# Kernel optimization log

Measured on AMD Instinct MI355X. Metric: run time of the kernel, lower is better.

## Reference

```python
import jax, jax.numpy as jnp
import numpy as np

NUM_HEADS = 8


def _mc_linear(x, W, b):
    # Per-channel linear over the feature (h) dim.
    # x: (b,c,h,w), W: (c,f,h), b: (c,f,1) -> (b,c,f,w)
    return jnp.einsum('bchw,cfh->bcfw', x, W) + b


def setup_inputs() -> dict:
    key = jax.random.key(0)
    ks = jax.random.split(key, 9)
    b, c, f, w = 2, 8, 256, 1024
    s = 1.0 / np.sqrt(f).astype(np.float32)
    d = {'x': jax.random.normal(ks[0], (b, c, f, w), jnp.float32)}
    for i, name in enumerate(['q', 'k', 'v', 'o']):
        d['W' + name] = jax.random.normal(ks[1 + 2 * i], (c, f, f), jnp.float32) * s
        d['b' + name] = jax.random.normal(ks[2 + 2 * i], (c, f, 1), jnp.float32) * 0.01
    return d


def reference(x, Wq, bq, Wk, bk, Wv, bv, Wo, bo):
    b, c, h, w = x.shape
    hd = h // NUM_HEADS
    # projections -> (b,c,f,w), then to (b,c,heads,w,hd) / (b,c,heads,hd,w)
    q = _mc_linear(x, Wq, bq).transpose(0, 1, 3, 2).reshape(b, c, w, NUM_HEADS, hd).transpose(0, 1, 3, 2, 4)
    k = _mc_linear(x, Wk, bk).transpose(0, 1, 3, 2).reshape(b, c, w, NUM_HEADS, hd).transpose(0, 1, 3, 4, 2)
    v = _mc_linear(x, Wv, bv).transpose(0, 1, 3, 2).reshape(b, c, w, NUM_HEADS, hd).transpose(0, 1, 3, 2, 4)
    qk = jnp.matmul(q, k) / jnp.sqrt(jnp.asarray(h, x.dtype))  # (b,c,heads,w,w); note scale uses h, per source
    a = jnp.matmul(jax.nn.softmax(qk, axis=-1), v)             # (b,c,heads,w,hd)
    a = a.transpose(0, 1, 3, 2, 4).reshape(b, c, w, h).transpose(0, 1, 3, 2)  # (b,c,h,w)
    out = _mc_linear(a, Wo, bo)
    return out, qk
```

## Files before the change

kernel.cpp:

```cpp
#include <hip/hip_runtime.h>
#include <hip/hip_bf16.h>

#define BC 16
#define HH 256
#define WW 1024
#define NH 8
#define HD 32
#define SST 68

typedef __attribute__((ext_vector_type(8))) short bf16x8;
typedef __attribute__((ext_vector_type(4))) float f32x4;

static __device__ __forceinline__ unsigned short f2bu(float f) {
    __hip_bfloat16 h = __float2bfloat16(f);
    unsigned short r;
    __builtin_memcpy(&r, &h, 2);
    return r;
}

__global__ __launch_bounds__(256) void cast_fused(
    const float* __restrict__ x, __hip_bfloat16* __restrict__ xT,
    const float* __restrict__ w0, const float* __restrict__ w1,
    const float* __restrict__ w2, const float* __restrict__ w3,
    __hip_bfloat16* __restrict__ o0, __hip_bfloat16* __restrict__ o1,
    __hip_bfloat16* __restrict__ o2, __hip_bfloat16* __restrict__ o3) {
    if (blockIdx.z == 16) {
        const float* src = w0;
        __hip_bfloat16* dst = o0;
        if (blockIdx.y == 1) { src = w1; dst = o1; }
        else if (blockIdx.y == 2) { src = w2; dst = o2; }
        else if (blockIdx.y == 3) { src = w3; dst = o3; }
        const int base = blockIdx.x * 256 + threadIdx.x;
#pragma unroll
        for (int i = 0; i < 32; ++i) {
            const long t = (long)base + (long)i * 4096;
            float4 v = ((const float4*)src)[t];
            ushort4 o = make_ushort4(f2bu(v.x), f2bu(v.y), f2bu(v.z), f2bu(v.w));
            ((ushort4*)dst)[t] = o;
        }
        return;
    }
    __shared__ float tile[64][65];
    const int bc = blockIdx.z;
    const int h0 = blockIdx.y * 64, w0t = blockIdx.x * 64;
    const int tx = threadIdx.x & 63, ty = threadIdx.x >> 6;
    const float* xp = x + ((long)bc * HH + h0) * WW + w0t;
    for (int r = ty; r < 64; r += 4)
        tile[r][tx] = xp[(long)r * WW + tx];
    __syncthreads();
    __hip_bfloat16* xo = xT + ((long)bc * WW + w0t) * HH + h0;
    for (int r = ty; r < 64; r += 4)
        xo[(long)r * HH + tx] = __float2bfloat16(tile[tx][r]);
}

template <int MI, int NI, int OUTF32>
static __device__ __forceinline__ void gemm_body(
    const __hip_bfloat16* __restrict__ Ap, int lda,
    const __hip_bfloat16* __restrict__ Bp, int ldb,
    char* __restrict__ Cp, int ldc,
    const float* __restrict__ bp, int biasMode, int m0, int n0, int lane) {
    const int lr = lane & 15, kl = (lane >> 4) * 8;

    const __hip_bfloat16* ap = Ap + (long)(m0 + lr) * lda + kl;
    const __hip_bfloat16* bpp = Bp + (long)(n0 + lr) * ldb + kl;

    f32x4 acc[MI][NI] = {};
    bf16x8 afA[MI], bfA[NI], afB[MI], bfB[NI];
#pragma unroll
    for (int i = 0; i < MI; ++i) afA[i] = *(const bf16x8*)(ap + (long)i * 16 * lda);
#pragma unroll
    for (int j = 0; j < NI; ++j) bfA[j] = *(const bf16x8*)(bpp + (long)j * 16 * ldb);

#pragma unroll
    for (int kk = 0; kk < 8; ++kk) {
        const int kn = (kk + 1) * 32;
        if ((kk & 1) == 0) {
            if (kn < HH) {
#pragma unroll
                for (int i = 0; i < MI; ++i)
                    afB[i] = *(const bf16x8*)(ap + (long)i * 16 * lda + kn);
#pragma unroll
                for (int j = 0; j < NI; ++j)
                    bfB[j] = *(const bf16x8*)(bpp + (long)j * 16 * ldb + kn);
            }
#pragma unroll
            for (int i = 0; i < MI; ++i)
#pragma unroll
                for (int j = 0; j < NI; ++j)
                    acc[i][j] = __builtin_amdgcn_mfma_f32_16x16x32_bf16(
                        afA[i], bfA[j], acc[i][j], 0, 0, 0);
        } else {
            if (kn < HH) {
#pragma unroll
                for (int i = 0; i < MI; ++i)
                    afA[i] = *(const bf16x8*)(ap + (long)i * 16 * lda + kn);
#pragma unroll
                for (int j = 0; j < NI; ++j)
                    bfA[j] = *(const bf16x8*)(bpp + (long)j * 16 * ldb + kn);
            }
#pragma unroll
            for (int i = 0; i < MI; ++i)
#pragma unroll
                for (int j = 0; j < NI; ++j)
                    acc[i][j] = __builtin_amdgcn_mfma_f32_16x16x32_bf16(
                        afB[i], bfB[j], acc[i][j], 0, 0, 0);
        }
    }

    const int col0 = lane & 15;
    const int rowg = (lane >> 4) * 4;
#pragma unroll
    for (int i = 0; i < MI; ++i) {
#pragma unroll
        for (int j = 0; j < NI; ++j) {
            const int n = n0 + j * 16 + col0;
            float addc = 0.0f;
            if (biasMode == 2) addc = bp[n];
#pragma unroll
            for (int r = 0; r < 4; ++r) {
                const int m = m0 + i * 16 + rowg + r;
                float v = acc[i][j][r] + ((biasMode == 1) ? bp[m] : addc);
                if (OUTF32)
                    ((float*)Cp)[(long)m * ldc + n] = v;
                else
                    ((__hip_bfloat16*)Cp)[(long)m * ldc + n] = __float2bfloat16(v);
            }
        }
    }
}

__global__ __launch_bounds__(256, 3) void gemm_qkv(
    const __hip_bfloat16* __restrict__ xT,
    const __hip_bfloat16* __restrict__ wqb, const __hip_bfloat16* __restrict__ wkb,
    const __hip_bfloat16* __restrict__ wvb,
    __hip_bfloat16* __restrict__ Qt, __hip_bfloat16* __restrict__ Kt,
    __hip_bfloat16* __restrict__ Vm,
    const float* __restrict__ bq, const float* __restrict__ bk,
    const float* __restrict__ bv) {
    const int bc = blockIdx.z, ch = bc & 7, y = blockIdx.y;
    const int wave = threadIdx.x >> 6, lane = threadIdx.x & 63;
    const __hip_bfloat16* xb = xT + (long)bc * WW * HH;

    if (y < 2) {
        const __hip_bfloat16* wb = ((y == 0) ? wqb : wkb) + (long)ch * HH * HH;
        __hip_bfloat16* Cb = ((y == 0) ? Qt : Kt) + (long)bc * WW * HH;
        const float* bp = ((y == 0) ? bq : bk) + ch * HH;
        const int bm = (blockIdx.x >> 1) * 128, bn = (blockIdx.x & 1) * 128;
        const int m0 = bm + (wave >> 1) * 64, n0 = bn + (wave & 1) * 64;
        gemm_body<4, 4, 0>(xb, HH, wb, HH, (char*)Cb, HH, bp, 2, m0, n0, lane);
    } else {
        const __hip_bfloat16* wb = wvb + (long)ch * HH * HH;
        __hip_bfloat16* Cb = Vm + (long)bc * HH * WW;
        const float* bp = bv + ch * HH;
        const int bm = (blockIdx.x >> 3) * 128, bn = (blockIdx.x & 7) * 128;
        const int m0 = bm + (wave >> 1) * 64, n0 = bn + (wave & 1) * 64;
        gemm_body<4, 4, 0>(wb, HH, xb, HH, (char*)Cb, WW, bp, 1, m0, n0, lane);
    }
}

__global__ __launch_bounds__(256, 2) void gemm_o(
    const __hip_bfloat16* __restrict__ wob, const __hip_bfloat16* __restrict__ At,
    float* __restrict__ out, const float* __restrict__ bo) {
    const int bc = blockIdx.z, ch = bc & 7;
    const int wave = threadIdx.x >> 6, lane = threadIdx.x & 63;
    const __hip_bfloat16* wb = wob + (long)ch * HH * HH;
    const __hip_bfloat16* ab = At + (long)bc * WW * HH;
    float* Cb = out + (long)bc * HH * WW;
    const float* bp = bo + ch * HH;
    const int bm = (blockIdx.x >> 4) * 128, bn = (blockIdx.x & 15) * 64;
    const int m0 = bm + (wave >> 1) * 64, n0 = bn + (wave & 1) * 32;
    gemm_body<4, 2, 1>(wb, HH, ab, HH, (char*)Cb, WW, bp, 1, m0, n0, lane);
}

static __device__ __forceinline__ void attn_body(
    const bf16x8 (&kc)[4], const bf16x8 (&vc)[2][2],
    bf16x8 (&kn)[4], bf16x8 (&vn)[2][2], bool pre, int wj,
    const bf16x8 (&qf)[2], float* __restrict__ sl, float* __restrict__ qkp,
    const __hip_bfloat16* __restrict__ Kb, const __hip_bfloat16* __restrict__ Vb,
    f32x4 (&oacc)[2][2], float (&lacc)[2],
    int lr, int g, int kl, int rowg) {
    const f32x4 zf = {0.0f, 0.0f, 0.0f, 0.0f};
    f32x4 s[2][4];
#pragma unroll
    for (int mf = 0; mf < 2; ++mf)
#pragma unroll
        for (int nf = 0; nf < 4; ++nf)
            s[mf][nf] = __builtin_amdgcn_mfma_f32_16x16x32_bf16(
                qf[mf], kc[nf], zf, 0, 0, 0);

#pragma unroll
    for (int mf = 0; mf < 2; ++mf)
#pragma unroll
        for (int nf = 0; nf < 4; ++nf) {
            s[mf][nf] *= 0.0625f;
#pragma unroll
            for (int r = 0; r < 4; ++r)
                sl[(mf * 16 + rowg + r) * SST + nf * 16 + lr] = s[mf][nf][r];
        }

    f32x4 sd[8];
#pragma unroll
    for (int st = 0; st < 8; ++st)
        sd[st] = *(const f32x4*)(sl + (st * 4 + g) * SST + lr * 4);

    if (pre) {
#pragma unroll
        for (int nf = 0; nf < 4; ++nf)
            kn[nf] = *(const bf16x8*)(Kb + (long)(wj + 64 + nf * 16 + lr) * HH);
#pragma unroll
        for (int ks = 0; ks < 2; ++ks)
#pragma unroll
            for (int nf = 0; nf < 2; ++nf)
                vn[ks][nf] = *(const bf16x8*)(Vb + (long)(nf * 16 + lr) * WW +
                                              wj + 64 + ks * 32 + kl);
    }

#pragma unroll
    for (int st = 0; st < 8; ++st)
        __builtin_nontemporal_store(
            sd[st], (f32x4*)(qkp + (long)(st * 4 + g) * WW + wj + lr * 4));

#pragma unroll
    for (int ks = 0; ks < 2; ++ks) {
        bf16x8 pf[2];
#pragma unroll
        for (int mf = 0; mf < 2; ++mf) {
            const float* sr = sl + (mf * 16 + lr) * SST + ks * 32 + kl;
            f32x4 a = *(const f32x4*)(sr);
            f32x4 b = *(const f32x4*)(sr + 4);
            float p[8];
#pragma unroll
            for (int j = 0; j < 4; ++j) p[j] = __expf(a[j]);
#pragma unroll
            for (int j = 0; j < 4; ++j) p[4 + j] = __expf(b[j]);
            float sum = 0.0f;
            bf16x8 pv;
#pragma unroll
            for (int j = 0; j < 8; ++j) {
                sum += p[j];
                pv[j] = (short)f2bu(p[j]);
            }
            lacc[mf] += sum;
            pf[mf] = pv;
        }
#pragma unroll
        for (int mf = 0; mf < 2; ++mf)
#pragma unroll
            for (int nf = 0; nf < 2; ++nf)
                oacc[mf][nf] = __builtin_amdgcn_mfma_f32_16x16x32_bf16(
                    pf[mf], vc[ks][nf], oacc[mf][nf], 0, 0, 0);
    }
}

__global__ __launch_bounds__(256) void attn_fused(
    const __hip_bfloat16* __restrict__ Qt, const __hip_bfloat16* __restrict__ Kt,
    const __hip_bfloat16* __restrict__ Vm, float* __restrict__ qk_out,
    __hip_bfloat16* __restrict__ At) {
    __shared__ float S_lds[4][32 * SST];
    const int bc = blockIdx.z, head = blockIdx.y;
    const int wave = threadIdx.x >> 6, lane = threadIdx.x & 63;
    const int wi0 = blockIdx.x * 128 + wave * 32;
    const int lr = lane & 15, g = lane >> 4, kl = g * 8;
    const int rowg = g * 4;

    const __hip_bfloat16* Qb = Qt + (long)bc * WW * HH;
    bf16x8 qf[2];
#pragma unroll
    for (int mf = 0; mf < 2; ++mf)
        qf[mf] = *(const bf16x8*)(Qb + (long)(wi0 + mf * 16 + lr) * HH + head * HD + kl);

    const __hip_bfloat16* Kb = Kt + (long)bc * WW * HH + head * HD + kl;
    const __hip_bfloat16* Vb = Vm + ((long)bc * HH + head * HD) * WW;
    float* qkp = qk_out + (((long)bc * NH + head) * WW + wi0) * WW;

    f32x4 oacc[2][2] = {};
    float lacc[2] = {0.0f, 0.0f};
    float* sl = &S_lds[wave][0];

    bf16x8 kfA[4], kfB[4], vfA[2][2], vfB[2][2];
#pragma unroll
    for (int nf = 0; nf < 4; ++nf)
        kfA[nf] = *(const bf16x8*)(Kb + (long)(nf * 16 + lr) * HH);
#pragma unroll
    for (int ks = 0; ks < 2; ++ks)
#pragma unroll
        for (int nf = 0; nf < 2; ++nf)
            vfA[ks][nf] = *(const bf16x8*)(Vb + (long)(nf * 16 + lr) * WW +
                                           ks * 32 + kl);

    for (int it = 0; it < 8; ++it) {
        const int wj0 = it * 128;
        attn_body(kfA, vfA, kfB, vfB, true, wj0,
                  qf, sl, qkp, Kb, Vb, oacc, lacc, lr, g, kl, rowg);
        attn_body(kfB, vfB, kfA, vfA, (it < 7), wj0 + 64,
                  qf, sl, qkp, Kb, Vb, oacc, lacc, lr, g, kl, rowg);
    }

#pragma unroll
    for (int mf = 0; mf < 2; ++mf) {
        lacc[mf] += __shfl_xor(lacc[mf], 16);
        lacc[mf] += __shfl_xor(lacc[mf], 32);
    }
    float linv[2][4];
#pragma unroll
    for (int mf = 0; mf < 2; ++mf)
#pragma unroll
        for (int r = 0; r < 4; ++r)
            linv[mf][r] = 1.0f / __shfl(lacc[mf], rowg + r);

    __hip_bfloat16* Ao = At + (long)bc * WW * HH;
#pragma unroll
    for (int mf = 0; mf < 2; ++mf)
#pragma unroll
        for (int nf = 0; nf < 2; ++nf)
#pragma unroll
            for (int r = 0; r < 4; ++r) {
                float v = oacc[mf][nf][r] * linv[mf][r];
                Ao[(long)(wi0 + mf * 16 + rowg + r) * HH + head * HD + nf * 16 + lr] =
                    __float2bfloat16(v);
            }
}

extern "C" void kernel_launch(void* const* d_in, const int* in_sizes, int n_in,
                              void* d_out, int out_size, void* d_ws, size_t ws_size,
                              hipStream_t stream) {
    const float* x  = (const float*)d_in[0];
    const float* Wq = (const float*)d_in[1];
    const float* bq = (const float*)d_in[2];
    const float* Wk = (const float*)d_in[3];
    const float* bk = (const float*)d_in[4];
    const float* Wv = (const float*)d_in[5];
    const float* bv = (const float*)d_in[6];
    const float* Wo = (const float*)d_in[7];
    const float* bo = (const float*)d_in[8];

    float* out = (float*)d_out;
    float* qk  = out + (long)BC * HH * WW;

    char* ws = (char*)d_ws;
    __hip_bfloat16* xT  = (__hip_bfloat16*)(ws);
    __hip_bfloat16* wqb = (__hip_bfloat16*)(ws + 8388608);
    __hip_bfloat16* wkb = (__hip_bfloat16*)(ws + 9437184);
    __hip_bfloat16* wvb = (__hip_bfloat16*)(ws + 10485760);
    __hip_bfloat16* wob = (__hip_bfloat16*)(ws + 11534336);
    __hip_bfloat16* Qt  = (__hip_bfloat16*)(ws + 12582912);
    __hip_bfloat16* Kt  = (__hip_bfloat16*)(ws + 20971520);
    __hip_bfloat16* Vm  = (__hip_bfloat16*)(ws + 29360128);
    __hip_bfloat16* At  = (__hip_bfloat16*)(ws + 37748736);

    cast_fused<<<dim3(16, 4, 17), 256, 0, stream>>>(
        x, xT, Wq, Wk, Wv, Wo, wqb, wkb, wvb, wob);

    gemm_qkv<<<dim3(16, 3, BC), 256, 0, stream>>>(
        xT, wqb, wkb, wvb, Qt, Kt, Vm, bq, bk, bv);

    attn_fused<<<dim3(8, NH, BC), 256, 0, stream>>>(Qt, Kt, Vm, qk, At);

    gemm_o<<<dim3(32, 1, BC), 256, 0, stream>>>(wob, At, out, bo);

    (void)in_sizes; (void)n_in; (void)out_size; (void)ws_size;
}
```

Measured before the change: 190.4 us.

## Fold softmax scale into Wq, store bf16 P to LDS, vectorize transpose

```diff
diff --git a/kernel.cpp b/kernel.cpp
--- a/kernel.cpp
+++ b/kernel.cpp
@@ -6,7 +6,7 @@
 #define WW 1024
 #define NH 8
 #define HD 32
-#define SST 68
+#define PST 72
 
 typedef __attribute__((ext_vector_type(8))) short bf16x8;
 typedef __attribute__((ext_vector_type(4))) float f32x4;
@@ -27,15 +27,17 @@
     if (blockIdx.z == 16) {
         const float* src = w0;
         __hip_bfloat16* dst = o0;
-        if (blockIdx.y == 1) { src = w1; dst = o1; }
-        else if (blockIdx.y == 2) { src = w2; dst = o2; }
-        else if (blockIdx.y == 3) { src = w3; dst = o3; }
+        float wscale = 0.0625f;
+        if (blockIdx.y == 1) { src = w1; dst = o1; wscale = 1.0f; }
+        else if (blockIdx.y == 2) { src = w2; dst = o2; wscale = 1.0f; }
+        else if (blockIdx.y == 3) { src = w3; dst = o3; wscale = 1.0f; }
         const int base = blockIdx.x * 256 + threadIdx.x;
 #pragma unroll
         for (int i = 0; i < 32; ++i) {
             const long t = (long)base + (long)i * 4096;
             float4 v = ((const float4*)src)[t];
-            ushort4 o = make_ushort4(f2bu(v.x), f2bu(v.y), f2bu(v.z), f2bu(v.w));
+            ushort4 o = make_ushort4(f2bu(v.x * wscale), f2bu(v.y * wscale),
+                                     f2bu(v.z * wscale), f2bu(v.w * wscale));
             ((ushort4*)dst)[t] = o;
         }
         return;
@@ -43,14 +45,27 @@
     __shared__ float tile[64][65];
     const int bc = blockIdx.z;
     const int h0 = blockIdx.y * 64, w0t = blockIdx.x * 64;
-    const int tx = threadIdx.x & 63, ty = threadIdx.x >> 6;
     const float* xp = x + ((long)bc * HH + h0) * WW + w0t;
-    for (int r = ty; r < 64; r += 4)
-        tile[r][tx] = xp[(long)r * WW + tx];
+    const int w4 = threadIdx.x & 15, hr = threadIdx.x >> 4;
+#pragma unroll
+    for (int p = 0; p < 4; ++p) {
+        const int h = hr + p * 16;
+        float4 v = *(const float4*)(xp + (long)h * WW + w4 * 4);
+        tile[h][w4 * 4 + 0] = v.x;
+        tile[h][w4 * 4 + 1] = v.y;
+        tile[h][w4 * 4 + 2] = v.z;
+        tile[h][w4 * 4 + 3] = v.w;
+    }
     __syncthreads();
     __hip_bfloat16* xo = xT + ((long)bc * WW + w0t) * HH + h0;
-    for (int r = ty; r < 64; r += 4)
-        xo[(long)r * HH + tx] = __float2bfloat16(tile[tx][r]);
+    const int hq = threadIdx.x & 15, wq = threadIdx.x >> 4;
+#pragma unroll
+    for (int p = 0; p < 4; ++p) {
+        const int w = wq + p * 16;
+        ushort4 o = make_ushort4(f2bu(tile[hq * 4 + 0][w]), f2bu(tile[hq * 4 + 1][w]),
+                                 f2bu(tile[hq * 4 + 2][w]), f2bu(tile[hq * 4 + 3][w]));
+        *(ushort4*)(xo + (long)w * HH + hq * 4) = o;
+    }
 }
 
 template <int MI, int NI, int OUTF32>
@@ -58,7 +73,8 @@
     const __hip_bfloat16* __restrict__ Ap, int lda,
     const __hip_bfloat16* __restrict__ Bp, int ldb,
     char* __restrict__ Cp, int ldc,
-    const float* __restrict__ bp, int biasMode, int m0, int n0, int lane) {
+    const float* __restrict__ bp, int biasMode, float bmul,
+    int m0, int n0, int lane) {
     const int lr = lane & 15, kl = (lane >> 4) * 8;
 
     const __hip_bfloat16* ap = Ap + (long)(m0 + lr) * lda + kl;
@@ -115,7 +131,7 @@
         for (int j = 0; j < NI; ++j) {
             const int n = n0 + j * 16 + col0;
             float addc = 0.0f;
-            if (biasMode == 2) addc = bp[n];
+            if (biasMode == 2) addc = bp[n] * bmul;
 #pragma unroll
             for (int r = 0; r < 4; ++r) {
                 const int m = m0 + i * 16 + rowg + r;
@@ -145,16 +161,17 @@
         const __hip_bfloat16* wb = ((y == 0) ? wqb : wkb) + (long)ch * HH * HH;
         __hip_bfloat16* Cb = ((y == 0) ? Qt : Kt) + (long)bc * WW * HH;
         const float* bp = ((y == 0) ? bq : bk) + ch * HH;
+        const float bmul = (y == 0) ? 0.0625f : 1.0f;
         const int bm = (blockIdx.x >> 1) * 128, bn = (blockIdx.x & 1) * 128;
         const int m0 = bm + (wave >> 1) * 64, n0 = bn + (wave & 1) * 64;
-        gemm_body<4, 4, 0>(xb, HH, wb, HH, (char*)Cb, HH, bp, 2, m0, n0, lane);
+        gemm_body<4, 4, 0>(xb, HH, wb, HH, (char*)Cb, HH, bp, 2, bmul, m0, n0, lane);
     } else {
         const __hip_bfloat16* wb = wvb + (long)ch * HH * HH;
         __hip_bfloat16* Cb = Vm + (long)bc * HH * WW;
         const float* bp = bv + ch * HH;
         const int bm = (blockIdx.x >> 3) * 128, bn = (blockIdx.x & 7) * 128;
         const int m0 = bm + (wave >> 1) * 64, n0 = bn + (wave & 1) * 64;
-        gemm_body<4, 4, 0>(wb, HH, xb, HH, (char*)Cb, WW, bp, 1, m0, n0, lane);
+        gemm_body<4, 4, 0>(wb, HH, xb, HH, (char*)Cb, WW, bp, 1, 1.0f, m0, n0, lane);
     }
 }
 
@@ -169,15 +186,16 @@
     const float* bp = bo + ch * HH;
     const int bm = (blockIdx.x >> 4) * 128, bn = (blockIdx.x & 15) * 64;
     const int m0 = bm + (wave >> 1) * 64, n0 = bn + (wave & 1) * 32;
-    gemm_body<4, 2, 1>(wb, HH, ab, HH, (char*)Cb, WW, bp, 1, m0, n0, lane);
+    gemm_body<4, 2, 1>(wb, HH, ab, HH, (char*)Cb, WW, bp, 1, 1.0f, m0, n0, lane);
 }
 
 static __device__ __forceinline__ void attn_body(
     const bf16x8 (&kc)[4], const bf16x8 (&vc)[2][2],
     bf16x8 (&kn)[4], bf16x8 (&vn)[2][2], bool pre, int wj,
-    const bf16x8 (&qf)[2], float* __restrict__ sl, float* __restrict__ qkp,
+    const bf16x8 (&qf)[2], __hip_bfloat16* __restrict__ pl,
+    float* __restrict__ qkp,
     const __hip_bfloat16* __restrict__ Kb, const __hip_bfloat16* __restrict__ Vb,
-    f32x4 (&oacc)[2][2], float (&lacc)[2],
+    f32x4 (&oacc)[2][2], float (&lacc)[2][4],
     int lr, int g, int kl, int rowg) {
     const f32x4 zf = {0.0f, 0.0f, 0.0f, 0.0f};
     f32x4 s[2][4];
@@ -188,21 +206,6 @@
             s[mf][nf] = __builtin_amdgcn_mfma_f32_16x16x32_bf16(
                 qf[mf], kc[nf], zf, 0, 0, 0);
 
-#pragma unroll
-    for (int mf = 0; mf < 2; ++mf)
-#pragma unroll
-        for (int nf = 0; nf < 4; ++nf) {
-            s[mf][nf] *= 0.0625f;
-#pragma unroll
-            for (int r = 0; r < 4; ++r)
-                sl[(mf * 16 + rowg + r) * SST + nf * 16 + lr] = s[mf][nf][r];
-        }
-
-    f32x4 sd[8];
-#pragma unroll
-    for (int st = 0; st < 8; ++st)
-        sd[st] = *(const f32x4*)(sl + (st * 4 + g) * SST + lr * 4);
-
     if (pre) {
 #pragma unroll
         for (int nf = 0; nf < 4; ++nf)
@@ -216,33 +219,34 @@
     }
 
 #pragma unroll
-    for (int st = 0; st < 8; ++st)
-        __builtin_nontemporal_store(
-            sd[st], (f32x4*)(qkp + (long)(st * 4 + g) * WW + wj + lr * 4));
+    for (int mf = 0; mf < 2; ++mf)
+#pragma unroll
+        for (int r = 0; r < 4; ++r) {
+            float* qr = qkp + (long)(mf * 16 + rowg + r) * WW + wj + lr;
+#pragma unroll
+            for (int nf = 0; nf < 4; ++nf)
+                __builtin_nontemporal_store(s[mf][nf][r], qr + nf * 16);
+        }
+
+#pragma unroll
+    for (int mf = 0; mf < 2; ++mf) {
+        __hip_bfloat16* pw = pl + (long)(mf * 16 + rowg) * PST + lr;
+#pragma unroll
+        for (int nf = 0; nf < 4; ++nf)
+#pragma unroll
+            for (int r = 0; r < 4; ++r) {
+                float p = __expf(s[mf][nf][r]);
+                lacc[mf][r] += p;
+                pw[r * PST + nf * 16] = __float2bfloat16(p);
+            }
+    }
 
 #pragma unroll
     for (int ks = 0; ks < 2; ++ks) {
         bf16x8 pf[2];
 #pragma unroll
-        for (int mf = 0; mf < 2; ++mf) {
-            const float* sr = sl + (mf * 16 + lr) * SST + ks * 32 + kl;
-            f32x4 a = *(const f32x4*)(sr);
-            f32x4 b = *(const f32x4*)(sr + 4);
-            float p[8];
-#pragma unroll
-            for (int j = 0; j < 4; ++j) p[j] = __expf(a[j]);
-#pragma unroll
-            for (int j = 0; j < 4; ++j) p[4 + j] = __expf(b[j]);
-            float sum = 0.0f;
-            bf16x8 pv;
-#pragma unroll
-            for (int j = 0; j < 8; ++j) {
-                sum += p[j];
-                pv[j] = (short)f2bu(p[j]);
-            }
-            lacc[mf] += sum;
-            pf[mf] = pv;
-        }
+        for (int mf = 0; mf < 2; ++mf)
+            pf[mf] = *(const bf16x8*)(pl + (long)(mf * 16 + lr) * PST + ks * 32 + kl);
 #pragma unroll
         for (int mf = 0; mf < 2; ++mf)
 #pragma unroll
@@ -256,7 +260,7 @@
     const __hip_bfloat16* __restrict__ Qt, const __hip_bfloat16* __restrict__ Kt,
     const __hip_bfloat16* __restrict__ Vm, float* __restrict__ qk_out,
     __hip_bfloat16* __restrict__ At) {
-    __shared__ float S_lds[4][32 * SST];
+    __shared__ __hip_bfloat16 P_lds[4][32 * PST];
     const int bc = blockIdx.z, head = blockIdx.y;
     const int wave = threadIdx.x >> 6, lane = threadIdx.x & 63;
     const int wi0 = blockIdx.x * 128 + wave * 32;
@@ -274,8 +278,8 @@
     float* qkp = qk_out + (((long)bc * NH + head) * WW + wi0) * WW;
 
     f32x4 oacc[2][2] = {};
-    float lacc[2] = {0.0f, 0.0f};
-    float* sl = &S_lds[wave][0];
+    float lacc[2][4] = {};
+    __hip_bfloat16* pl = &P_lds[wave][0];
 
     bf16x8 kfA[4], kfB[4], vfA[2][2], vfB[2][2];
 #pragma unroll
@@ -291,22 +295,23 @@
     for (int it = 0; it < 8; ++it) {
         const int wj0 = it * 128;
         attn_body(kfA, vfA, kfB, vfB, true, wj0,
-                  qf, sl, qkp, Kb, Vb, oacc, lacc, lr, g, kl, rowg);
+                  qf, pl, qkp, Kb, Vb, oacc, lacc, lr, g, kl, rowg);
         attn_body(kfB, vfB, kfA, vfA, (it < 7), wj0 + 64,
-                  qf, sl, qkp, Kb, Vb, oacc, lacc, lr, g, kl, rowg);
-    }
-
-#pragma unroll
-    for (int mf = 0; mf < 2; ++mf) {
-        lacc[mf] += __shfl_xor(lacc[mf], 16);
-        lacc[mf] += __shfl_xor(lacc[mf], 32);
-    }
+                  qf, pl, qkp, Kb, Vb, oacc, lacc, lr, g, kl, rowg);
+    }
+
     float linv[2][4];
 #pragma unroll
     for (int mf = 0; mf < 2; ++mf)
 #pragma unroll
-        for (int r = 0; r < 4; ++r)
-            linv[mf][r] = 1.0f / __shfl(lacc[mf], rowg + r);
+        for (int r = 0; r < 4; ++r) {
+            float v = lacc[mf][r];
+            v += __shfl_xor(v, 1);
+            v += __shfl_xor(v, 2);
+            v += __shfl_xor(v, 4);
+            v += __shfl_xor(v, 8);
+            linv[mf][r] = 1.0f / v;
+        }
 
     __hip_bfloat16* Ao = At + (long)bc * WW * HH;
 #pragma unroll
```

Result: slower. 200.7 us (+5.4%).

## Fuse fp32-to-bf16 casts into GEMM fragment loads and drop cast kernel

Applied to the files above, without the earlier changes.

```diff
diff --git a/kernel.cpp b/kernel.cpp
--- a/kernel.cpp
+++ b/kernel.cpp
@@ -18,58 +18,46 @@
     return r;
 }
 
-__global__ __launch_bounds__(256) void cast_fused(
-    const float* __restrict__ x, __hip_bfloat16* __restrict__ xT,
-    const float* __restrict__ w0, const float* __restrict__ w1,
-    const float* __restrict__ w2, const float* __restrict__ w3,
-    __hip_bfloat16* __restrict__ o0, __hip_bfloat16* __restrict__ o1,
-    __hip_bfloat16* __restrict__ o2, __hip_bfloat16* __restrict__ o3) {
-    if (blockIdx.z == 16) {
-        const float* src = w0;
-        __hip_bfloat16* dst = o0;
-        if (blockIdx.y == 1) { src = w1; dst = o1; }
-        else if (blockIdx.y == 2) { src = w2; dst = o2; }
-        else if (blockIdx.y == 3) { src = w3; dst = o3; }
-        const int base = blockIdx.x * 256 + threadIdx.x;
-#pragma unroll
-        for (int i = 0; i < 32; ++i) {
-            const long t = (long)base + (long)i * 4096;
-            float4 v = ((const float4*)src)[t];
-            ushort4 o = make_ushort4(f2bu(v.x), f2bu(v.y), f2bu(v.z), f2bu(v.w));
-            ((ushort4*)dst)[t] = o;
-        }
-        return;
-    }
-    __shared__ float tile[64][65];
-    const int bc = blockIdx.z;
-    const int h0 = blockIdx.y * 64, w0t = blockIdx.x * 64;
-    const int tx = threadIdx.x & 63, ty = threadIdx.x >> 6;
-    const float* xp = x + ((long)bc * HH + h0) * WW + w0t;
-    for (int r = ty; r < 64; r += 4)
-        tile[r][tx] = xp[(long)r * WW + tx];
-    __syncthreads();
-    __hip_bfloat16* xo = xT + ((long)bc * WW + w0t) * HH + h0;
-    for (int r = ty; r < 64; r += 4)
-        xo[(long)r * HH + tx] = __float2bfloat16(tile[tx][r]);
-}
-
-template <int MI, int NI, int OUTF32>
+template <int LK>
+static __device__ __forceinline__ bf16x8 load_frag(
+    const void* __restrict__ p, long row, int k, int ld, float scale) {
+    bf16x8 r;
+    if constexpr (LK == 0) {
+        r = *(const bf16x8*)((const __hip_bfloat16*)p + row * (long)ld + k);
+    } else if constexpr (LK == 1) {
+        const float* f = (const float*)p + row * (long)ld + k;
+        float4 a = *(const float4*)f;
+        float4 b = *(const float4*)(f + 4);
+        r[0] = (short)f2bu(a.x * scale); r[1] = (short)f2bu(a.y * scale);
+        r[2] = (short)f2bu(a.z * scale); r[3] = (short)f2bu(a.w * scale);
+        r[4] = (short)f2bu(b.x * scale); r[5] = (short)f2bu(b.y * scale);
+        r[6] = (short)f2bu(b.z * scale); r[7] = (short)f2bu(b.w * scale);
+    } else {
+        const float* f = (const float*)p + row + (long)k * ld;
+#pragma unroll
+        for (int j = 0; j < 8; ++j)
+            r[j] = (short)f2bu(f[(long)j * ld]);
+    }
+    return r;
+}
+
+template <int MI, int NI, int OUTF32, int LKA, int LKB>
 static __device__ __forceinline__ void gemm_body(
-    const __hip_bfloat16* __restrict__ Ap, int lda,
-    const __hip_bfloat16* __restrict__ Bp, int ldb,
+    const void* __restrict__ Ap, int lda, float asc,
+    const void* __restrict__ Bp, int ldb, float bsc,
     char* __restrict__ Cp, int ldc,
-    const float* __restrict__ bp, int biasMode, int m0, int n0, int lane) {
+    const float* __restrict__ bp, int biasMode, float bmul,
+    int m0, int n0, int lane) {
     const int lr = lane & 15, kl = (lane >> 4) * 8;
-
-    const __hip_bfloat16* ap = Ap + (long)(m0 + lr) * lda + kl;
-    const __hip_bfloat16* bpp = Bp + (long)(n0 + lr) * ldb + kl;
 
     f32x4 acc[MI][NI] = {};
     bf16x8 afA[MI], bfA[NI], afB[MI], bfB[NI];
 #pragma unroll
-    for (int i = 0; i < MI; ++i) afA[i] = *(const bf16x8*)(ap + (long)i * 16 * lda);
-#pragma unroll
-    for (int j = 0; j < NI; ++j) bfA[j] = *(const bf16x8*)(bpp + (long)j * 16 * ldb);
+    for (int i = 0; i < MI; ++i)
+        afA[i] = load_frag<LKA>(Ap, m0 + i * 16 + lr, kl, lda, asc);
+#pragma unroll
+    for (int j = 0; j < NI; ++j)
+        bfA[j] = load_frag<LKB>(Bp, n0 + j * 16 + lr, kl, ldb, bsc);
 
 #pragma unroll
     for (int kk = 0; kk < 8; ++kk) {
@@ -78,10 +66,10 @@
             if (kn < HH) {
 #pragma unroll
                 for (int i = 0; i < MI; ++i)
-                    afB[i] = *(const bf16x8*)(ap + (long)i * 16 * lda + kn);
+                    afB[i] = load_frag<LKA>(Ap, m0 + i * 16 + lr, kl + kn, lda, asc);
 #pragma unroll
                 for (int j = 0; j < NI; ++j)
-                    bfB[j] = *(const bf16x8*)(bpp + (long)j * 16 * ldb + kn);
+                    bfB[j] = load_frag<LKB>(Bp, n0 + j * 16 + lr, kl + kn, ldb, bsc);
             }
 #pragma unroll
             for (int i = 0; i < MI; ++i)
@@ -93,10 +81,10 @@
             if (kn < HH) {
 #pragma unroll
                 for (int i = 0; i < MI; ++i)
-                    afA[i] = *(const bf16x8*)(ap + (long)i * 16 * lda + kn);
+                    afA[i] = load_frag<LKA>(Ap, m0 + i * 16 + lr, kl + kn, lda, asc);
 #pragma unroll
                 for (int j = 0; j < NI; ++j)
-                    bfA[j] = *(const bf16x8*)(bpp + (long)j * 16 * ldb + kn);
+                    bfA[j] = load_frag<LKB>(Bp, n0 + j * 16 + lr, kl + kn, ldb, bsc);
             }
 #pragma unroll
             for (int i = 0; i < MI; ++i)
@@ -115,7 +103,7 @@
         for (int j = 0; j < NI; ++j) {
             const int n = n0 + j * 16 + col0;
             float addc = 0.0f;
-            if (biasMode == 2) addc = bp[n];
+            if (biasMode == 2) addc = bp[n] * bmul;
 #pragma unroll
             for (int r = 0; r < 4; ++r) {
                 const int m = m0 + i * 16 + rowg + r;
@@ -130,46 +118,57 @@
 }
 
 __global__ __launch_bounds__(256, 3) void gemm_qkv(
-    const __hip_bfloat16* __restrict__ xT,
-    const __hip_bfloat16* __restrict__ wqb, const __hip_bfloat16* __restrict__ wkb,
-    const __hip_bfloat16* __restrict__ wvb,
+    const float* __restrict__ x,
+    const float* __restrict__ Wq, const float* __restrict__ Wk,
+    const float* __restrict__ Wv,
     __hip_bfloat16* __restrict__ Qt, __hip_bfloat16* __restrict__ Kt,
     __hip_bfloat16* __restrict__ Vm,
     const float* __restrict__ bq, const float* __restrict__ bk,
     const float* __restrict__ bv) {
     const int bc = blockIdx.z, ch = bc & 7, y = blockIdx.y;
     const int wave = threadIdx.x >> 6, lane = threadIdx.x & 63;
-    const __hip_bfloat16* xb = xT + (long)bc * WW * HH;
-
-    if (y < 2) {
-        const __hip_bfloat16* wb = ((y == 0) ? wqb : wkb) + (long)ch * HH * HH;
-        __hip_bfloat16* Cb = ((y == 0) ? Qt : Kt) + (long)bc * WW * HH;
-        const float* bp = ((y == 0) ? bq : bk) + ch * HH;
+    const float* xb = x + (long)bc * HH * WW;
+
+    if (y == 0) {
+        const float* wb = Wq + (long)ch * HH * HH;
+        __hip_bfloat16* Cb = Qt + (long)bc * WW * HH;
         const int bm = (blockIdx.x >> 1) * 128, bn = (blockIdx.x & 1) * 128;
         const int m0 = bm + (wave >> 1) * 64, n0 = bn + (wave & 1) * 64;
-        gemm_body<4, 4, 0>(xb, HH, wb, HH, (char*)Cb, HH, bp, 2, m0, n0, lane);
+        gemm_body<4, 4, 0, 2, 1>(xb, WW, 1.0f, wb, HH, 0.0625f,
+                                 (char*)Cb, HH, bq + ch * HH, 2, 0.0625f,
+                                 m0, n0, lane);
+    } else if (y == 1) {
+        const float* wb = Wk + (long)ch * HH * HH;
+        __hip_bfloat16* Cb = Kt + (long)bc * WW * HH;
+        const int bm = (blockIdx.x >> 1) * 128, bn = (blockIdx.x & 1) * 128;
+        const int m0 = bm + (wave >> 1) * 64, n0 = bn + (wave & 1) * 64;
+        gemm_body<4, 4, 0, 2, 1>(xb, WW, 1.0f, wb, HH, 1.0f,
+                                 (char*)Cb, HH, bk + ch * HH, 2, 1.0f,
+                                 m0, n0, lane);
     } else {
-        const __hip_bfloat16* wb = wvb + (long)ch * HH * HH;
+        const float* wb = Wv + (long)ch * HH * HH;
         __hip_bfloat16* Cb = Vm + (long)bc * HH * WW;
-        const float* bp = bv + ch * HH;
         const int bm = (blockIdx.x >> 3) * 128, bn = (blockIdx.x & 7) * 128;
         const int m0 = bm + (wave >> 1) * 64, n0 = bn + (wave & 1) * 64;
-        gemm_body<4, 4, 0>(wb, HH, xb, HH, (char*)Cb, WW, bp, 1, m0, n0, lane);
+        gemm_body<4, 4, 0, 1, 2>(wb, HH, 1.0f, xb, WW, 1.0f,
+                                 (char*)Cb, WW, bv + ch * HH, 1, 1.0f,
+                                 m0, n0, lane);
     }
 }
 
 __global__ __launch_bounds__(256, 2) void gemm_o(
-    const __hip_bfloat16* __restrict__ wob, const __hip_bfloat16* __restrict__ At,
+    const float* __restrict__ Wo, const __hip_bfloat16* __restrict__ At,
     float* __restrict__ out, const float* __restrict__ bo) {
     const int bc = blockIdx.z, ch = bc & 7;
     const int wave = threadIdx.x >> 6, lane = threadIdx.x & 63;
-    const __hip_bfloat16* wb = wob + (long)ch * HH * HH;
+    const float* wb = Wo + (long)ch * HH * HH;
     const __hip_bfloat16* ab = At + (long)bc * WW * HH;
     float* Cb = out + (long)bc * HH * WW;
     const float* bp = bo + ch * HH;
     const int bm = (blockIdx.x >> 4) * 128, bn = (blockIdx.x & 15) * 64;
     const int m0 = bm + (wave >> 1) * 64, n0 = bn + (wave & 1) * 32;
-    gemm_body<4, 2, 1>(wb, HH, ab, HH, (char*)Cb, WW, bp, 1, m0, n0, lane);
+    gemm_body<4, 2, 1, 1, 0>(wb, HH, 1.0f, ab, HH, 1.0f,
+                             (char*)Cb, WW, bp, 1, 1.0f, m0, n0, lane);
 }
 
 static __device__ __forceinline__ void attn_body(
@@ -192,7 +191,6 @@
     for (int mf = 0; mf < 2; ++mf)
 #pragma unroll
         for (int nf = 0; nf < 4; ++nf) {
-            s[mf][nf] *= 0.0625f;
 #pragma unroll
             for (int r = 0; r < 4; ++r)
                 sl[(mf * 16 + rowg + r) * SST + nf * 16 + lr] = s[mf][nf][r];
@@ -338,25 +336,17 @@
     float* qk  = out + (long)BC * HH * WW;
 
     char* ws = (char*)d_ws;
-    __hip_bfloat16* xT  = (__hip_bfloat16*)(ws);
-    __hip_bfloat16* wqb = (__hip_bfloat16*)(ws + 8388608);
-    __hip_bfloat16* wkb = (__hip_bfloat16*)(ws + 9437184);
-    __hip_bfloat16* wvb = (__hip_bfloat16*)(ws + 10485760);
-    __hip_bfloat16* wob = (__hip_bfloat16*)(ws + 11534336);
-    __hip_bfloat16* Qt  = (__hip_bfloat16*)(ws + 12582912);
-    __hip_bfloat16* Kt  = (__hip_bfloat16*)(ws + 20971520);
-    __hip_bfloat16* Vm  = (__hip_bfloat16*)(ws + 29360128);
-    __hip_bfloat16* At  = (__hip_bfloat16*)(ws + 37748736);
-
-    cast_fused<<<dim3(16, 4, 17), 256, 0, stream>>>(
-        x, xT, Wq, Wk, Wv, Wo, wqb, wkb, wvb, wob);
+    __hip_bfloat16* Qt = (__hip_bfloat16*)(ws);
+    __hip_bfloat16* Kt = (__hip_bfloat16*)(ws + 8388608);
+    __hip_bfloat16* Vm = (__hip_bfloat16*)(ws + 16777216);
+    __hip_bfloat16* At = (__hip_bfloat16*)(ws + 25165824);
 
     gemm_qkv<<<dim3(16, 3, BC), 256, 0, stream>>>(
-        xT, wqb, wkb, wvb, Qt, Kt, Vm, bq, bk, bv);
+        x, Wq, Wk, Wv, Qt, Kt, Vm, bq, bk, bv);
 
     attn_fused<<<dim3(8, NH, BC), 256, 0, stream>>>(Qt, Kt, Vm, qk, At);
 
-    gemm_o<<<dim3(32, 1, BC), 256, 0, stream>>>(wob, At, out, bo);
+    gemm_o<<<dim3(32, 1, BC), 256, 0, stream>>>(Wo, At, out, bo);
 
     (void)in_sizes; (void)n_in; (void)out_size; (void)ws_size;
 }
```

New measurement: 202.6 us. 6.4% more time.
